# Kernel optimization log

Hardware: AMD Instinct MI355X
Metric: run time of the kernel (lower is better)

## Reference

```python
import jax, jax.numpy as jnp
import numpy as np

B, T, C = 2, 2048, 2048
H = 16
HD = C // H
MLP_DIM = 4 * C
EPS = 1e-5


def rmsnorm(x):
    return x * jax.lax.rsqrt(jnp.mean(x * x, axis=-1, keepdims=True) + EPS)


def setup_inputs() -> dict:
    key = jax.random.key(0)
    ks = jax.random.split(key, 7)
    s = 0.02
    return {
        "x": jax.random.normal(ks[0], (B, T, C), dtype=jnp.float32),
        "wq": jax.random.normal(ks[1], (C, C), dtype=jnp.float32) * s,
        "wk": jax.random.normal(ks[2], (C, C), dtype=jnp.float32) * s,
        "wv": jax.random.normal(ks[3], (C, C), dtype=jnp.float32) * s,
        "wo": jax.random.normal(ks[4], (C, C), dtype=jnp.float32) * s,
        "fc1": jax.random.normal(ks[5], (MLP_DIM, C), dtype=jnp.float32) * s,
        "fc2": jax.random.normal(ks[6], (C, MLP_DIM), dtype=jnp.float32) * s,
    }


def reference(x, wq, wk, wv, wo, fc1, fc2):
    # --- attention sub-block (pre-norm) ---
    h = rmsnorm(x)
    # nn.Linear applies x @ W.T
    q = (h @ wq.T).reshape(B, T, H, HD).transpose(0, 2, 1, 3)  # [B,H,T,HD]
    k = (h @ wk.T).reshape(B, T, H, HD).transpose(0, 2, 1, 3)
    v = (h @ wv.T).reshape(B, T, H, HD).transpose(0, 2, 1, 3)
    scale = 1.0 / np.sqrt(HD)
    scores = jnp.einsum("bhqd,bhkd->bhqk", q, k) * scale
    causal_mask = jnp.triu(jnp.full((T, T), -jnp.inf, dtype=scores.dtype), k=1)
    scores = scores + causal_mask
    attn = jax.nn.softmax(scores, axis=-1)
    out = jnp.einsum("bhqk,bhkd->bhqd", attn, v)
    out = out.transpose(0, 2, 1, 3).reshape(B, T, C)
    x = x + out @ wo.T
    # --- MLP sub-block (squared ReLU) ---
    h = rmsnorm(x)
    m = h @ fc1.T
    m = jnp.square(jax.nn.relu(m))
    x = x + m @ fc2.T
    return x
```

## Files before the change

### kernel.cpp

```cpp
#include <hip/hip_runtime.h>


typedef __bf16 bf16x8 __attribute__((ext_vector_type(8)));
typedef __bf16 bf16x4 __attribute__((ext_vector_type(4)));
typedef float  f32x4  __attribute__((ext_vector_type(4)));

static __device__ __forceinline__ __bf16 tobf(float f) { return (__bf16)f; }

static __device__ __forceinline__ void async_copy16(const void* g, void* l) {
    __builtin_amdgcn_global_load_lds(
        (const __attribute__((address_space(1))) void*)g,
        (__attribute__((address_space(3))) void*)l, 16, 0, 0);
}

#define LGKM0_FENCE()  asm volatile("s_waitcnt lgkmcnt(0)" ::: "memory")
#define VMCNT8_FENCE() asm volatile("s_waitcnt vmcnt(8)" ::: "memory")

__global__ void detect_dtype_kernel(const unsigned short* __restrict__ xh,
                                    int* __restrict__ flag) {
    int t = threadIdx.x;
    unsigned short u = xh[2 * t];
    int e = (u >> 7) & 0xFF;
    bool outlier = (e < 100) || (e > 131);
    unsigned long long m = __ballot(outlier);
    if (t == 0) *flag = (__popcll(m) >= 16) ? 1 : 0;
}

__global__ __launch_bounds__(256) void convert_w4(
    const void* __restrict__ w0, const void* __restrict__ w1,
    const void* __restrict__ w2, const void* __restrict__ w3,
    __bf16* __restrict__ dqkvo, const int* __restrict__ flagp) {
    constexpr size_t CC = (size_t)2048 * 2048;
    const int y = blockIdx.y;
    size_t i = ((size_t)blockIdx.x * 256 + threadIdx.x) * 8;
    const void* s = (y == 0) ? w0 : (y == 1) ? w1 : (y == 2) ? w2 : w3;
    __bf16* d = dqkvo + (size_t)y * CC;
    if (*flagp != 0) {
        const float4* sp = (const float4*)((const float*)s + i);
        float4 a = sp[0], b = sp[1];
        bf16x8 o = {tobf(a.x), tobf(a.y), tobf(a.z), tobf(a.w),
                    tobf(b.x), tobf(b.y), tobf(b.z), tobf(b.w)};
        *(bf16x8*)(d + i) = o;
    } else {
        *(bf16x8*)(d + i) = *(const bf16x8*)((const __bf16*)s + i);
    }
}

__global__ __launch_bounds__(256) void convert_w1(
    const void* __restrict__ src, __bf16* __restrict__ dst,
    const int* __restrict__ flagp) {
    size_t i = ((size_t)blockIdx.x * 256 + threadIdx.x) * 8;
    if (*flagp != 0) {
        const float4* sp = (const float4*)((const float*)src + i);
        float4 a = sp[0], b = sp[1];
        bf16x8 o = {tobf(a.x), tobf(a.y), tobf(a.z), tobf(a.w),
                    tobf(b.x), tobf(b.y), tobf(b.z), tobf(b.w)};
        *(bf16x8*)(dst + i) = o;
    } else {
        *(bf16x8*)(dst + i) = *(const bf16x8*)((const __bf16*)src + i);
    }
}

template <int SRC>
__global__ __launch_bounds__(256) void rmsnorm_kernel(
    const void* __restrict__ xp, __bf16* __restrict__ h,
    const int* __restrict__ flagp) {
    constexpr int C = 2048;
    const int row = blockIdx.x, t = threadIdx.x;
    float vals[8];
    bool f32in = (SRC == 1) || (*flagp != 0);
    if (f32in) {
        const float4* xr = (const float4*)((const float*)xp + (size_t)row * C);
        float4 a = xr[2 * t], b = xr[2 * t + 1];
        vals[0] = a.x; vals[1] = a.y; vals[2] = a.z; vals[3] = a.w;
        vals[4] = b.x; vals[5] = b.y; vals[6] = b.z; vals[7] = b.w;
    } else {
        bf16x8 a = *((const bf16x8*)((const __bf16*)xp + (size_t)row * C) + t);
#pragma unroll
        for (int j = 0; j < 8; ++j) vals[j] = (float)a[j];
    }
    float ss = 0.f;
#pragma unroll
    for (int j = 0; j < 8; ++j) ss += vals[j] * vals[j];
#pragma unroll
    for (int off = 32; off > 0; off >>= 1) ss += __shfl_down(ss, off);
    __shared__ float red[4];
    if ((t & 63) == 0) red[t >> 6] = ss;
    __syncthreads();
    float mean = (red[0] + red[1] + red[2] + red[3]) * (1.0f / C);
    float sc = rsqrtf(mean + 1e-5f);
    bf16x8 o;
#pragma unroll
    for (int j = 0; j < 8; ++j) o[j] = tobf(vals[j] * sc);
    *((bf16x8*)(h + (size_t)row * C) + t) = o;
}

static __device__ __forceinline__ void gemm_core_256(
    const __bf16* __restrict__ A, const __bf16* __restrict__ W,
    int m0, int n0, int K,
    __bf16 (*As)[256][64], __bf16 (*Bs)[256][64], f32x4 (&acc)[8][4]) {
    const int tid = threadIdx.x;
    const int wave = tid >> 6, lane = tid & 63;
    const int lr = lane & 15, lq = lane >> 4;
    const int wm = wave >> 2, wn = wave & 3;
    const int sx = lr & 7;
    const int NT = K >> 6;

    int off[4], lo[4];
#pragma unroll
    for (int i = 0; i < 4; ++i) {
        int c = i * 512 + tid;
        int row = c >> 3;
        off[i] = row * K + (((c & 7) ^ (row & 7)) * 8);
        lo[i] = (c & ~63) * 8;
    }

    const f32x4 zero = {0.f, 0.f, 0.f, 0.f};
#pragma unroll
    for (int m = 0; m < 8; ++m)
#pragma unroll
        for (int n = 0; n < 4; ++n) acc[m][n] = zero;

#pragma unroll
    for (int pt = 0; pt < 2; ++pt) {
        const __bf16* ga = A + (size_t)m0 * K + pt * 64;
        const __bf16* gb = W + (size_t)n0 * K + pt * 64;
#pragma unroll
        for (int i = 0; i < 4; ++i)
            async_copy16(ga + off[i], &As[pt][0][0] + lo[i]);
#pragma unroll
        for (int i = 0; i < 4; ++i)
            async_copy16(gb + off[i], &Bs[pt][0][0] + lo[i]);
    }
    VMCNT8_FENCE();
    __builtin_amdgcn_s_barrier();

    for (int t = 0; t < NT; ++t) {
        const int bi = t & 1;
        const __bf16 (*Ac)[64] = As[bi];
        const __bf16 (*Bc)[64] = Bs[bi];
        const int ts = (t + 2 < NT) ? t + 2 : NT - 1;
        const __bf16* gAt = A + (size_t)m0 * K + (size_t)ts * 64;
        const __bf16* gBt = W + (size_t)n0 * K + (size_t)ts * 64;

        bf16x8 a0[4][2], a1[4][2], b0[2][2], b1[2][2];

#pragma unroll
        for (int m = 0; m < 4; ++m)
#pragma unroll
            for (int kk = 0; kk < 2; ++kk)
                a0[m][kk] = *(const bf16x8*)
                    &Ac[wm * 128 + m * 16 + lr][((kk * 4 + lq) ^ sx) * 8];
#pragma unroll
        for (int n = 0; n < 2; ++n)
#pragma unroll
            for (int kk = 0; kk < 2; ++kk)
                b0[n][kk] = *(const bf16x8*)
                    &Bc[wn * 64 + n * 16 + lr][((kk * 4 + lq) ^ sx) * 8];
        __builtin_amdgcn_s_barrier();
        LGKM0_FENCE();
        __builtin_amdgcn_s_setprio(1);
#pragma unroll
        for (int m = 0; m < 4; ++m)
#pragma unroll
            for (int n = 0; n < 2; ++n)
#pragma unroll
                for (int kk = 0; kk < 2; ++kk)
                    acc[m][n] = __builtin_amdgcn_mfma_f32_16x16x32_bf16(
                        a0[m][kk], b0[n][kk], acc[m][n], 0, 0, 0);
        __builtin_amdgcn_s_setprio(0);
        __builtin_amdgcn_s_barrier();

#pragma unroll
        for (int m = 0; m < 4; ++m)
#pragma unroll
            for (int kk = 0; kk < 2; ++kk)
                a1[m][kk] = *(const bf16x8*)
                    &Ac[wm * 128 + (m + 4) * 16 + lr][((kk * 4 + lq) ^ sx) * 8];
        __builtin_amdgcn_s_barrier();
        LGKM0_FENCE();
        __builtin_amdgcn_s_setprio(1);
#pragma unroll
        for (int m = 0; m < 4; ++m)
#pragma unroll
            for (int n = 0; n < 2; ++n)
#pragma unroll
                for (int kk = 0; kk < 2; ++kk)
                    acc[m + 4][n] = __builtin_amdgcn_mfma_f32_16x16x32_bf16(
                        a1[m][kk], b0[n][kk], acc[m + 4][n], 0, 0, 0);
        __builtin_amdgcn_s_setprio(0);
        __builtin_amdgcn_s_barrier();

#pragma unroll
        for (int n = 0; n < 2; ++n)
#pragma unroll
            for (int kk = 0; kk < 2; ++kk)
                b1[n][kk] = *(const bf16x8*)
                    &Bc[wn * 64 + (n + 2) * 16 + lr][((kk * 4 + lq) ^ sx) * 8];
#pragma unroll
        for (int i = 0; i < 4; ++i)
            async_copy16(gAt + off[i], &As[bi][0][0] + lo[i]);
        __builtin_amdgcn_s_barrier();
        LGKM0_FENCE();
        __builtin_amdgcn_s_setprio(1);
#pragma unroll
        for (int m = 0; m < 4; ++m)
#pragma unroll
            for (int n = 0; n < 2; ++n)
#pragma unroll
                for (int kk = 0; kk < 2; ++kk)
                    acc[m + 4][n + 2] = __builtin_amdgcn_mfma_f32_16x16x32_bf16(
                        a1[m][kk], b1[n][kk], acc[m + 4][n + 2], 0, 0, 0);
        __builtin_amdgcn_s_setprio(0);
        __builtin_amdgcn_s_barrier();

#pragma unroll
        for (int i = 0; i < 4; ++i)
            async_copy16(gBt + off[i], &Bs[bi][0][0] + lo[i]);
        __builtin_amdgcn_s_barrier();
        __builtin_amdgcn_s_setprio(1);
#pragma unroll
        for (int m = 0; m < 4; ++m)
#pragma unroll
            for (int n = 0; n < 2; ++n)
#pragma unroll
                for (int kk = 0; kk < 2; ++kk)
                    acc[m][n + 2] = __builtin_amdgcn_mfma_f32_16x16x32_bf16(
                        a0[m][kk], b1[n][kk], acc[m][n + 2], 0, 0, 0);
        __builtin_amdgcn_s_setprio(0);
        VMCNT8_FENCE();
        __builtin_amdgcn_s_barrier();
    }
}

template <int EPI>
__global__ __launch_bounds__(512, 1) void gemm256_nt(
    const __bf16* __restrict__ A, const __bf16* __restrict__ W,
    void* __restrict__ outp, const void* __restrict__ resp,
    int M, int N, int K, const int* __restrict__ flagp) {
    __shared__ __align__(16) __bf16 As[2][256][64];
    __shared__ __align__(16) __bf16 Bs[2][256][64];
    const int tid = threadIdx.x;
    const int wave = tid >> 6, lane = tid & 63;
    const int lr = lane & 15, lq = lane >> 4;
    const int wm = wave >> 2, wn = wave & 3;
    const int m0 = blockIdx.y * 256, n0 = blockIdx.x * 256;

    f32x4 acc[8][4];
    gemm_core_256(A, W, m0, n0, K, As, Bs, acc);

    const bool f32 = (EPI == 2) ? false : (*flagp != 0);
#pragma unroll
    for (int m = 0; m < 8; ++m)
#pragma unroll
        for (int n = 0; n < 4; ++n)
#pragma unroll
            for (int r = 0; r < 4; ++r) {
                int row = m0 + wm * 128 + m * 16 + lq * 4 + r;
                int col = n0 + wn * 64 + n * 16 + lr;
                size_t o = (size_t)row * N + col;
                float v = acc[m][n][r];
                if (EPI == 2) {
                    float rv = v > 0.f ? v : 0.f;
                    ((__bf16*)outp)[o] = tobf(rv * rv);
                } else if (EPI == 5) {
                    float res = f32 ? ((const float*)resp)[o]
                                    : (float)((const __bf16*)resp)[o];
                    ((float*)outp)[o] = v + res;
                } else {
                    float ov = v + ((const float*)resp)[o];
                    if (f32) ((float*)outp)[o] = ov;
                    else     ((__bf16*)outp)[o] = tobf(ov);
                }
            }
}

__global__ __launch_bounds__(512, 1) void gemm256_qkv(
    const __bf16* __restrict__ A, const __bf16* __restrict__ Wall,
    __bf16* __restrict__ qout, __bf16* __restrict__ kout,
    __bf16* __restrict__ vtout) {
    constexpr int N = 2048, K = 2048;
    constexpr float kQScale = 1.4426950408889634f * 0.08838834764831845f;
    __shared__ __align__(16) __bf16 As[2][256][64];
    __shared__ __align__(16) __bf16 Bs[2][256][64];
    const int tid = threadIdx.x;
    const int wave = tid >> 6, lane = tid & 63;
    const int lr = lane & 15, lq = lane >> 4;
    const int wm = wave >> 2, wn = wave & 3;
    const int which = blockIdx.x >> 3;
    const int m0 = blockIdx.y * 256, n0 = (blockIdx.x & 7) * 256;
    const __bf16* W = Wall + (size_t)which * N * K;

    f32x4 acc[8][4];
    gemm_core_256(A, W, m0, n0, K, As, Bs, acc);

    if (which < 2) {
        __bf16* outp = (which == 0) ? qout : kout;
        const float sc = (which == 0) ? kQScale : 1.0f;
#pragma unroll
        for (int m = 0; m < 8; ++m)
#pragma unroll
            for (int n = 0; n < 4; ++n)
#pragma unroll
                for (int r = 0; r < 4; ++r) {
                    int row = m0 + wm * 128 + m * 16 + lq * 4 + r;
                    int col = n0 + wn * 64 + n * 16 + lr;
                    outp[(size_t)row * N + col] = tobf(acc[m][n][r] * sc);
                }
    } else {
#pragma unroll
        for (int m = 0; m < 8; ++m)
#pragma unroll
            for (int n = 0; n < 4; ++n) {
                int t0 = m0 + wm * 128 + m * 16 + lq * 4;
                int b  = t0 >> 11, tt = t0 & 2047;
                int col = n0 + wn * 64 + n * 16 + lr;
                bf16x4 p = {tobf(acc[m][n][0]), tobf(acc[m][n][1]),
                            tobf(acc[m][n][2]), tobf(acc[m][n][3])};
                *(bf16x4*)(vtout + (((size_t)(b * 2048 + col)) << 11) + tt) = p;
            }
    }
}

static __device__ __forceinline__ void gemm_core_128(
    const __bf16* __restrict__ A, const __bf16* __restrict__ W,
    int m0, int n0, int K,
    __bf16 (*As)[64], __bf16 (*Bs)[64], f32x4 (&acc)[4][4]) {
    const int t = threadIdx.x;
    const int wave = t >> 6, lane = t & 63;
    const int lr = lane & 15, lq = lane >> 4;
    const int wm = wave & 1, wn = wave >> 1;

    const __bf16* gA[4];
    const __bf16* gB[4];
    int lo[4];
#pragma unroll
    for (int i = 0; i < 4; ++i) {
        int c = i * 256 + t;
        int row = c >> 3;
        int sl = (c & 7) ^ (row & 7);
        gA[i] = A + (size_t)(m0 + row) * K + sl * 8;
        gB[i] = W + (size_t)(n0 + row) * K + sl * 8;
        lo[i] = (c & ~63) * 8;
    }
    const int sx = lr & 7;

    const f32x4 zero = {0.f, 0.f, 0.f, 0.f};
#pragma unroll
    for (int i = 0; i < 4; ++i)
#pragma unroll
        for (int j = 0; j < 4; ++j) acc[i][j] = zero;

    for (int k0 = 0; k0 < K; k0 += 64) {
#pragma unroll
        for (int i = 0; i < 4; ++i) {
            async_copy16(gA[i] + k0, &As[0][0] + lo[i]);
            async_copy16(gB[i] + k0, &Bs[0][0] + lo[i]);
        }
        __syncthreads();
#pragma unroll
        for (int kk = 0; kk < 2; ++kk) {
            const int sp = ((kk * 4 + lq) ^ sx) * 8;
            bf16x8 a[4], b[4];
#pragma unroll
            for (int ii = 0; ii < 4; ++ii) {
                a[ii] = *(const bf16x8*)&As[wm * 64 + ii * 16 + lr][sp];
                b[ii] = *(const bf16x8*)&Bs[wn * 64 + ii * 16 + lr][sp];
            }
#pragma unroll
            for (int ii = 0; ii < 4; ++ii)
#pragma unroll
                for (int jj = 0; jj < 4; ++jj)
                    acc[ii][jj] = __builtin_amdgcn_mfma_f32_16x16x32_bf16(
                        a[ii], b[jj], acc[ii][jj], 0, 0, 0);
        }
        __syncthreads();
    }
}

template <int EPI>
__global__ __launch_bounds__(256) void gemm_nt(
    const __bf16* __restrict__ A, const __bf16* __restrict__ W,
    void* __restrict__ outp, const void* __restrict__ resp,
    int M, int N, int K, const int* __restrict__ flagp) {
    __shared__ __align__(16) __bf16 As[128][64];
    __shared__ __align__(16) __bf16 Bs[128][64];
    const int t = threadIdx.x;
    const int wave = t >> 6, lane = t & 63;
    const int lr = lane & 15, lq = lane >> 4;
    const int wm = wave & 1, wn = wave >> 1;
    const int m0 = blockIdx.y * 128, n0 = blockIdx.x * 128;

    f32x4 acc[4][4];
    gemm_core_128(A, W, m0, n0, K, As, Bs, acc);

    const bool f32 = (*flagp != 0);
#pragma unroll
    for (int i = 0; i < 4; ++i)
#pragma unroll
        for (int j = 0; j < 4; ++j)
#pragma unroll
            for (int r = 0; r < 4; ++r) {
                int row = m0 + wm * 64 + i * 16 + lq * 4 + r;
                int col = n0 + wn * 64 + j * 16 + lr;
                size_t o = (size_t)row * N + col;
                float v = acc[i][j][r];
                if (EPI == 5) {
                    float res = f32 ? ((const float*)resp)[o]
                                    : (float)((const __bf16*)resp)[o];
                    ((float*)outp)[o] = v + res;
                } else {
                    float ov = v + ((const float*)resp)[o];
                    if (f32) ((float*)outp)[o] = ov;
                    else     ((__bf16*)outp)[o] = tobf(ov);
                }
            }
}

__global__ __launch_bounds__(256) void attn_kernel(
    const __bf16* __restrict__ Q, const __bf16* __restrict__ K,
    const __bf16* __restrict__ Vt, __bf16* __restrict__ O) {
    constexpr int T = 2048, C = 2048, HD = 128;
    __shared__ __align__(16) __bf16 Ks[64][136];
    __shared__ __align__(16) __bf16 Vts[128][72];
    __shared__ __align__(16) __bf16 Ps[4][16][72];
    const int t = threadIdx.x, w = t >> 6, lane = t & 63;
    const int lr = lane & 15, lq = lane >> 4;
    const int b = blockIdx.z, h = blockIdx.y;
    const __bf16* vtb = Vt + ((size_t)(b * 2048 + h * 128) << 11);
    const f32x4 zero = {0.f, 0.f, 0.f, 0.f};

    bf16x8 ones;
#pragma unroll
    for (int j = 0; j < 8; ++j) ones[j] = (lr == 0) ? (__bf16)1.0f : (__bf16)0.0f;

    for (int pass = 0; pass < 2; ++pass) {
        const int qblk = (pass == 0) ? blockIdx.x : 31 - blockIdx.x;
        const int q0 = qblk * 64;

        const int qrow = q0 + w * 16 + lr;
        const __bf16* qb = Q + (size_t)(b * T + qrow) * C + h * HD;
        bf16x8 qf[4];
#pragma unroll
        for (int s = 0; s < 4; ++s)
            qf[s] = *(const bf16x8*)(qb + s * 32 + lq * 8);

        f32x4 oacc[8], lacc = zero;
#pragma unroll
        for (int nc = 0; nc < 8; ++nc) oacc[nc] = zero;
        float m_i[4] = {-3e38f, -3e38f, -3e38f, -3e38f};

        for (int kb = 0; kb <= qblk; ++kb) {
            const int k00 = kb * 64;
#pragma unroll
            for (int i = 0; i < 4; ++i) {
                int c = t + 256 * i;
                int r = c >> 4, col = (c & 15) * 8;
                *(bf16x8*)&Ks[r][col] =
                    *(const bf16x8*)(K + (size_t)(b * T + k00 + r) * C + h * HD + col);
            }
#pragma unroll
            for (int i = 0; i < 4; ++i) {
                int c = t + 256 * i;
                int r = c >> 3, cg = (c & 7) * 8;
                *(bf16x8*)&Vts[r][cg] =
                    *(const bf16x8*)(vtb + ((size_t)r << 11) + k00 + cg);
            }
            __syncthreads();

            float pv[4][4];
#pragma unroll
            for (int jc = 0; jc < 4; ++jc) {
                f32x4 s = zero;
#pragma unroll
                for (int ks = 0; ks < 4; ++ks) {
                    bf16x8 kf = *(const bf16x8*)&Ks[jc * 16 + lr][ks * 32 + lq * 8];
                    s = __builtin_amdgcn_mfma_f32_16x16x32_bf16(qf[ks], kf, s, 0, 0, 0);
                }
#pragma unroll
                for (int r = 0; r < 4; ++r) pv[jc][r] = s[r];
            }
            if (kb == qblk) {
#pragma unroll
                for (int jc = 0; jc < 4; ++jc)
#pragma unroll
                    for (int r = 0; r < 4; ++r)
                        if (jc * 16 + lr > w * 16 + lq * 4 + r) pv[jc][r] = -3e38f;
            }
            float rmax[4];
#pragma unroll
            for (int r = 0; r < 4; ++r)
                rmax[r] = fmaxf(fmaxf(pv[0][r], pv[1][r]), fmaxf(pv[2][r], pv[3][r]));
#pragma unroll
            for (int off = 1; off < 16; off <<= 1)
#pragma unroll
                for (int r = 0; r < 4; ++r)
                    rmax[r] = fmaxf(rmax[r], __shfl_xor(rmax[r], off));
            float alpha[4];
#pragma unroll
            for (int r = 0; r < 4; ++r) {
                float mn = fmaxf(m_i[r], rmax[r]);
                alpha[r] = exp2f(m_i[r] - mn);
                m_i[r] = mn;
            }
#pragma unroll
            for (int jc = 0; jc < 4; ++jc)
#pragma unroll
                for (int r = 0; r < 4; ++r)
                    Ps[w][lq * 4 + r][jc * 16 + lr] = tobf(exp2f(pv[jc][r] - m_i[r]));
#pragma unroll
            for (int nc = 0; nc < 8; ++nc)
#pragma unroll
                for (int r = 0; r < 4; ++r) oacc[nc][r] *= alpha[r];
#pragma unroll
            for (int r = 0; r < 4; ++r) lacc[r] *= alpha[r];
            __syncthreads();

#pragma unroll
            for (int s2 = 0; s2 < 2; ++s2) {
                bf16x8 pa = *(const bf16x8*)&Ps[w][lr][s2 * 32 + lq * 8];
#pragma unroll
                for (int nc = 0; nc < 8; ++nc) {
                    bf16x8 vf = *(const bf16x8*)&Vts[nc * 16 + lr][s2 * 32 + lq * 8];
                    oacc[nc] = __builtin_amdgcn_mfma_f32_16x16x32_bf16(
                        pa, vf, oacc[nc], 0, 0, 0);
                }
                lacc = __builtin_amdgcn_mfma_f32_16x16x32_bf16(pa, ones, lacc, 0, 0, 0);
            }
            __syncthreads();
        }

        float inv[4];
#pragma unroll
        for (int r = 0; r < 4; ++r) inv[r] = 1.0f / __shfl(lacc[r], lane & 48);
#pragma unroll
        for (int nc = 0; nc < 8; ++nc)
#pragma unroll
            for (int r = 0; r < 4; ++r) {
                int row = q0 + w * 16 + lq * 4 + r;
                O[(size_t)(b * T + row) * C + h * HD + nc * 16 + lr] =
                    tobf(oacc[nc][r] * inv[r]);
            }
        __syncthreads();
    }
}

extern "C" void kernel_launch(void* const* d_in, const int* in_sizes, int n_in,
                              void* d_out, int out_size, void* d_ws, size_t ws_size,
                              hipStream_t stream) {
    const void* x   = d_in[0];
    const void* wq  = d_in[1];
    const void* wk  = d_in[2];
    const void* wv  = d_in[3];
    const void* wo  = d_in[4];
    const void* fc1 = d_in[5];
    const void* fc2 = d_in[6];
    constexpr int Bv = 2, Tv = 2048, Cv = 2048, Hv = 16, MLP = 8192;
    constexpr int M = Bv * Tv;
    constexpr size_t NE = (size_t)M * Cv;
    constexpr size_t CC = (size_t)Cv * Cv;

    char* ws = (char*)d_ws;
    int*    flag = (int*)ws;
    __bf16* h    = (__bf16*)(ws + 256);
    __bf16* qb   = h  + NE;
    __bf16* kb   = qb + NE;
    __bf16* vt   = kb + NE;
    __bf16* ao   = vt + NE;
    float*  x1   = (float*)(ao + NE);
    __bf16* mm   = (__bf16*)(x1 + NE);
    __bf16* wqkvob = mm;
    __bf16* fc1b   = qb;
    __bf16* fc2b   = vt;

    detect_dtype_kernel<<<1, 64, 0, stream>>>((const unsigned short*)x, flag);

    convert_w4<<<dim3(2048, 4), 256, 0, stream>>>(wq, wk, wv, wo, wqkvob, flag);

    rmsnorm_kernel<0><<<M, 256, 0, stream>>>(x, h, flag);

    gemm256_qkv<<<dim3(24, 16), 512, 0, stream>>>(h, wqkvob, qb, kb, vt);

    attn_kernel<<<dim3(16, Hv, Bv), 256, 0, stream>>>(qb, kb, vt, ao);

    convert_w1<<<8192, 256, 0, stream>>>(fc1, fc1b, flag);

    gemm_nt<5><<<dim3(16, 32), 256, 0, stream>>>(ao, wqkvob + 3 * CC, x1, x,
                                                 M, Cv, Cv, flag);

    convert_w1<<<8192, 256, 0, stream>>>(fc2, fc2b, flag);

    rmsnorm_kernel<1><<<M, 256, 0, stream>>>(x1, h, flag);

    gemm256_nt<2><<<dim3(32, 16), 512, 0, stream>>>(h, fc1b, mm, nullptr,
                                                    M, MLP, Cv, flag);

    gemm_nt<6><<<dim3(16, 32), 256, 0, stream>>>(mm, fc2b, d_out, x1,
                                                 M, Cv, MLP, flag);
}
```

Before: 800.8 us.

## Templatize 8-phase GEMM core and use 128x256 tiles for QKV, out-proj, fc2

Generalizes the pipelined 256x256 GEMM core into a template over the M tile height, so a 128x256 variant can share the same double-buffered async-copy and MFMA schedule. The QKV projection now uses 128x256 tiles, giving 768 blocks instead of 384 for better CU balance. The out-projection and fc2 GEMMs move from the simple single-buffered 128x128 kernel to this pipelined 128x256 kernel. The trade-off is less operand reuse per block than 256x256 and more blocks to schedule.

```diff
diff --git a/kernel.cpp b/kernel.cpp
--- a/kernel.cpp
+++ b/kernel.cpp
@@ -14,7 +14,6 @@
 }
 
 #define LGKM0_FENCE()  asm volatile("s_waitcnt lgkmcnt(0)" ::: "memory")
-#define VMCNT8_FENCE() asm volatile("s_waitcnt vmcnt(8)" ::: "memory")
 
 __global__ void detect_dtype_kernel(const unsigned short* __restrict__ xh,
                                     int* __restrict__ flag) {
@@ -95,10 +94,14 @@
     *((bf16x8*)(h + (size_t)row * C) + t) = o;
 }
 
-static __device__ __forceinline__ void gemm_core_256(
+template <int MH>
+static __device__ __forceinline__ void gemm_core_8ph(
     const __bf16* __restrict__ A, const __bf16* __restrict__ W,
-    int m0, int n0, int K,
-    __bf16 (*As)[256][64], __bf16 (*Bs)[256][64], f32x4 (&acc)[8][4]) {
+    int m0, int n0, int K, __bf16* __restrict__ AsB, __bf16* __restrict__ BsB,
+    f32x4 (&acc)[2 * MH][4]) {
+    constexpr int BM = 64 * MH;
+    constexpr int ASTRIDE = BM * 64;
+    constexpr int BSTRIDE = 256 * 64;
     const int tid = threadIdx.x;
     const int wave = tid >> 6, lane = tid & 63;
     const int lr = lane & 15, lq = lane >> 4;
@@ -106,18 +109,25 @@
     const int sx = lr & 7;
     const int NT = K >> 6;
 
-    int off[4], lo[4];
+    int offA[MH], loA[MH], offB[4], loB[4];
+#pragma unroll
+    for (int i = 0; i < MH; ++i) {
+        int c = i * 512 + tid;
+        int row = c >> 3;
+        offA[i] = row * K + (((c & 7) ^ (row & 7)) * 8);
+        loA[i] = (c & ~63) * 8;
+    }
 #pragma unroll
     for (int i = 0; i < 4; ++i) {
         int c = i * 512 + tid;
         int row = c >> 3;
-        off[i] = row * K + (((c & 7) ^ (row & 7)) * 8);
-        lo[i] = (c & ~63) * 8;
+        offB[i] = row * K + (((c & 7) ^ (row & 7)) * 8);
+        loB[i] = (c & ~63) * 8;
     }
 
     const f32x4 zero = {0.f, 0.f, 0.f, 0.f};
 #pragma unroll
-    for (int m = 0; m < 8; ++m)
+    for (int m = 0; m < 2 * MH; ++m)
 #pragma unroll
         for (int n = 0; n < 4; ++n) acc[m][n] = zero;
 
@@ -125,43 +135,46 @@
     for (int pt = 0; pt < 2; ++pt) {
         const __bf16* ga = A + (size_t)m0 * K + pt * 64;
         const __bf16* gb = W + (size_t)n0 * K + pt * 64;
-#pragma unroll
-        for (int i = 0; i < 4; ++i)
-            async_copy16(ga + off[i], &As[pt][0][0] + lo[i]);
-#pragma unroll
-        for (int i = 0; i < 4; ++i)
-            async_copy16(gb + off[i], &Bs[pt][0][0] + lo[i]);
-    }
-    VMCNT8_FENCE();
+        __bf16* la = AsB + pt * ASTRIDE;
+        __bf16* lb = BsB + pt * BSTRIDE;
+#pragma unroll
+        for (int i = 0; i < MH; ++i) async_copy16(ga + offA[i], la + loA[i]);
+#pragma unroll
+        for (int i = 0; i < 4; ++i)  async_copy16(gb + offB[i], lb + loB[i]);
+    }
+    if constexpr (MH == 4) asm volatile("s_waitcnt vmcnt(8)" ::: "memory");
+    else                   asm volatile("s_waitcnt vmcnt(6)" ::: "memory");
     __builtin_amdgcn_s_barrier();
 
     for (int t = 0; t < NT; ++t) {
         const int bi = t & 1;
-        const __bf16 (*Ac)[64] = As[bi];
-        const __bf16 (*Bc)[64] = Bs[bi];
+        const __bf16* Ac = AsB + bi * ASTRIDE;
+        const __bf16* Bc = BsB + bi * BSTRIDE;
         const int ts = (t + 2 < NT) ? t + 2 : NT - 1;
         const __bf16* gAt = A + (size_t)m0 * K + (size_t)ts * 64;
         const __bf16* gBt = W + (size_t)n0 * K + (size_t)ts * 64;
 
-        bf16x8 a0[4][2], a1[4][2], b0[2][2], b1[2][2];
-
-#pragma unroll
-        for (int m = 0; m < 4; ++m)
+        bf16x8 a0[MH][2], a1[MH][2], b0[2][2], b1[2][2];
+
+#pragma unroll
+        for (int m = 0; m < MH; ++m)
 #pragma unroll
             for (int kk = 0; kk < 2; ++kk)
                 a0[m][kk] = *(const bf16x8*)
-                    &Ac[wm * 128 + m * 16 + lr][((kk * 4 + lq) ^ sx) * 8];
+                    &Ac[(wm * (32 * MH) + m * 16 + lr) * 64 +
+                        ((kk * 4 + lq) ^ sx) * 8];
 #pragma unroll
         for (int n = 0; n < 2; ++n)
 #pragma unroll
             for (int kk = 0; kk < 2; ++kk)
                 b0[n][kk] = *(const bf16x8*)
-                    &Bc[wn * 64 + n * 16 + lr][((kk * 4 + lq) ^ sx) * 8];
+                    &Bc[(wn * 64 + n * 16 + lr) * 64 +
+                        ((kk * 4 + lq) ^ sx) * 8];
         __builtin_amdgcn_s_barrier();
         LGKM0_FENCE();
         __builtin_amdgcn_s_setprio(1);
 #pragma unroll
-        for (int m = 0; m < 4; ++m)
+        for (int m = 0; m < MH; ++m)
 #pragma unroll
             for (int n = 0; n < 2; ++n)
 #pragma unroll
@@ -172,22 +185,23 @@
         __builtin_amdgcn_s_barrier();
 
 #pragma unroll
-        for (int m = 0; m < 4; ++m)
+        for (int m = 0; m < MH; ++m)
 #pragma unroll
             for (int kk = 0; kk < 2; ++kk)
                 a1[m][kk] = *(const bf16x8*)
-                    &Ac[wm * 128 + (m + 4) * 16 + lr][((kk * 4 + lq) ^ sx) * 8];
+                    &Ac[(wm * (32 * MH) + (m + MH) * 16 + lr) * 64 +
+                        ((kk * 4 + lq) ^ sx) * 8];
         __builtin_amdgcn_s_barrier();
         LGKM0_FENCE();
         __builtin_amdgcn_s_setprio(1);
 #pragma unroll
-        for (int m = 0; m < 4; ++m)
+        for (int m = 0; m < MH; ++m)
 #pragma unroll
             for (int n = 0; n < 2; ++n)
 #pragma unroll
                 for (int kk = 0; kk < 2; ++kk)
-                    acc[m + 4][n] = __builtin_amdgcn_mfma_f32_16x16x32_bf16(
-                        a1[m][kk], b0[n][kk], acc[m + 4][n], 0, 0, 0);
+                    acc[m + MH][n] = __builtin_amdgcn_mfma_f32_16x16x32_bf16(
+                        a1[m][kk], b0[n][kk], acc[m + MH][n], 0, 0, 0);
         __builtin_amdgcn_s_setprio(0);
         __builtin_amdgcn_s_barrier();
 
@@ -196,31 +210,32 @@
 #pragma unroll
             for (int kk = 0; kk < 2; ++kk)
                 b1[n][kk] = *(const bf16x8*)
-                    &Bc[wn * 64 + (n + 2) * 16 + lr][((kk * 4 + lq) ^ sx) * 8];
-#pragma unroll
-        for (int i = 0; i < 4; ++i)
-            async_copy16(gAt + off[i], &As[bi][0][0] + lo[i]);
+                    &Bc[(wn * 64 + (n + 2) * 16 + lr) * 64 +
+                        ((kk * 4 + lq) ^ sx) * 8];
+#pragma unroll
+        for (int i = 0; i < MH; ++i)
+            async_copy16(gAt + offA[i], AsB + bi * ASTRIDE + loA[i]);
         __builtin_amdgcn_s_barrier();
         LGKM0_FENCE();
         __builtin_amdgcn_s_setprio(1);
 #pragma unroll
-        for (int m = 0; m < 4; ++m)
+        for (int m = 0; m < MH; ++m)
 #pragma unroll
             for (int n = 0; n < 2; ++n)
 #pragma unroll
                 for (int kk = 0; kk < 2; ++kk)
-                    acc[m + 4][n + 2] = __builtin_amdgcn_mfma_f32_16x16x32_bf16(
-                        a1[m][kk], b1[n][kk], acc[m + 4][n + 2], 0, 0, 0);
+                    acc[m + MH][n + 2] = __builtin_amdgcn_mfma_f32_16x16x32_bf16(
+                        a1[m][kk], b1[n][kk], acc[m + MH][n + 2], 0, 0, 0);
         __builtin_amdgcn_s_setprio(0);
         __builtin_amdgcn_s_barrier();
 
 #pragma unroll
         for (int i = 0; i < 4; ++i)
-            async_copy16(gBt + off[i], &Bs[bi][0][0] + lo[i]);
+            async_copy16(gBt + offB[i], BsB + bi * BSTRIDE + loB[i]);
         __builtin_amdgcn_s_barrier();
         __builtin_amdgcn_s_setprio(1);
 #pragma unroll
-        for (int m = 0; m < 4; ++m)
+        for (int m = 0; m < MH; ++m)
 #pragma unroll
             for (int n = 0; n < 2; ++n)
 #pragma unroll
@@ -228,7 +243,8 @@
                     acc[m][n + 2] = __builtin_amdgcn_mfma_f32_16x16x32_bf16(
                         a0[m][kk], b1[n][kk], acc[m][n + 2], 0, 0, 0);
         __builtin_amdgcn_s_setprio(0);
-        VMCNT8_FENCE();
+        if constexpr (MH == 4) asm volatile("s_waitcnt vmcnt(8)" ::: "memory");
+        else                   asm volatile("s_waitcnt vmcnt(6)" ::: "memory");
         __builtin_amdgcn_s_barrier();
     }
 }
@@ -247,7 +263,7 @@
     const int m0 = blockIdx.y * 256, n0 = blockIdx.x * 256;
 
     f32x4 acc[8][4];
-    gemm_core_256(A, W, m0, n0, K, As, Bs, acc);
+    gemm_core_8ph<4>(A, W, m0, n0, K, &As[0][0][0], &Bs[0][0][0], acc);
 
     const bool f32 = (EPI == 2) ? false : (*flagp != 0);
 #pragma unroll
@@ -275,136 +291,33 @@
             }
 }
 
-__global__ __launch_bounds__(512, 1) void gemm256_qkv(
-    const __bf16* __restrict__ A, const __bf16* __restrict__ Wall,
-    __bf16* __restrict__ qout, __bf16* __restrict__ kout,
-    __bf16* __restrict__ vtout) {
-    constexpr int N = 2048, K = 2048;
-    constexpr float kQScale = 1.4426950408889634f * 0.08838834764831845f;
-    __shared__ __align__(16) __bf16 As[2][256][64];
+template <int EPI>
+__global__ __launch_bounds__(512, 1) void gemm128_nt(
+    const __bf16* __restrict__ A, const __bf16* __restrict__ W,
+    void* __restrict__ outp, const void* __restrict__ resp,
+    int M, int N, int K, const int* __restrict__ flagp) {
+    __shared__ __align__(16) __bf16 As[2][128][64];
     __shared__ __align__(16) __bf16 Bs[2][256][64];
     const int tid = threadIdx.x;
     const int wave = tid >> 6, lane = tid & 63;
     const int lr = lane & 15, lq = lane >> 4;
     const int wm = wave >> 2, wn = wave & 3;
-    const int which = blockIdx.x >> 3;
-    const int m0 = blockIdx.y * 256, n0 = (blockIdx.x & 7) * 256;
-    const __bf16* W = Wall + (size_t)which * N * K;
-
-    f32x4 acc[8][4];
-    gemm_core_256(A, W, m0, n0, K, As, Bs, acc);
-
-    if (which < 2) {
-        __bf16* outp = (which == 0) ? qout : kout;
-        const float sc = (which == 0) ? kQScale : 1.0f;
-#pragma unroll
-        for (int m = 0; m < 8; ++m)
-#pragma unroll
-            for (int n = 0; n < 4; ++n)
-#pragma unroll
-                for (int r = 0; r < 4; ++r) {
-                    int row = m0 + wm * 128 + m * 16 + lq * 4 + r;
-                    int col = n0 + wn * 64 + n * 16 + lr;
-                    outp[(size_t)row * N + col] = tobf(acc[m][n][r] * sc);
-                }
-    } else {
-#pragma unroll
-        for (int m = 0; m < 8; ++m)
-#pragma unroll
-            for (int n = 0; n < 4; ++n) {
-                int t0 = m0 + wm * 128 + m * 16 + lq * 4;
-                int b  = t0 >> 11, tt = t0 & 2047;
+    const int m0 = blockIdx.y * 128, n0 = blockIdx.x * 256;
+
+    f32x4 acc[4][4];
+    gemm_core_8ph<2>(A, W, m0, n0, K, &As[0][0][0], &Bs[0][0][0], acc);
+
+    const bool f32 = (*flagp != 0);
+#pragma unroll
+    for (int m = 0; m < 4; ++m)
+#pragma unroll
+        for (int n = 0; n < 4; ++n)
+#pragma unroll
+            for (int r = 0; r < 4; ++r) {
+                int row = m0 + wm * 64 + m * 16 + lq * 4 + r;
                 int col = n0 + wn * 64 + n * 16 + lr;
-                bf16x4 p = {tobf(acc[m][n][0]), tobf(acc[m][n][1]),
-                            tobf(acc[m][n][2]), tobf(acc[m][n][3])};
-                *(bf16x4*)(vtout + (((size_t)(b * 2048 + col)) << 11) + tt) = p;
-            }
-    }
-}
-
-static __device__ __forceinline__ void gemm_core_128(
-    const __bf16* __restrict__ A, const __bf16* __restrict__ W,
-    int m0, int n0, int K,
-    __bf16 (*As)[64], __bf16 (*Bs)[64], f32x4 (&acc)[4][4]) {
-    const int t = threadIdx.x;
-    const int wave = t >> 6, lane = t & 63;
-    const int lr = lane & 15, lq = lane >> 4;
-    const int wm = wave & 1, wn = wave >> 1;
-
-    const __bf16* gA[4];
-    const __bf16* gB[4];
-    int lo[4];
-#pragma unroll
-    for (int i = 0; i < 4; ++i) {
-        int c = i * 256 + t;
-        int row = c >> 3;
-        int sl = (c & 7) ^ (row & 7);
-        gA[i] = A + (size_t)(m0 + row) * K + sl * 8;
-        gB[i] = W + (size_t)(n0 + row) * K + sl * 8;
-        lo[i] = (c & ~63) * 8;
-    }
-    const int sx = lr & 7;
-
-    const f32x4 zero = {0.f, 0.f, 0.f, 0.f};
-#pragma unroll
-    for (int i = 0; i < 4; ++i)
-#pragma unroll
-        for (int j = 0; j < 4; ++j) acc[i][j] = zero;
-
-    for (int k0 = 0; k0 < K; k0 += 64) {
-#pragma unroll
-        for (int i = 0; i < 4; ++i) {
-            async_copy16(gA[i] + k0, &As[0][0] + lo[i]);
-            async_copy16(gB[i] + k0, &Bs[0][0] + lo[i]);
-        }
-        __syncthreads();
-#pragma unroll
-        for (int kk = 0; kk < 2; ++kk) {
-            const int sp = ((kk * 4 + lq) ^ sx) * 8;
-            bf16x8 a[4], b[4];
-#pragma unroll
-            for (int ii = 0; ii < 4; ++ii) {
-                a[ii] = *(const bf16x8*)&As[wm * 64 + ii * 16 + lr][sp];
-                b[ii] = *(const bf16x8*)&Bs[wn * 64 + ii * 16 + lr][sp];
-            }
-#pragma unroll
-            for (int ii = 0; ii < 4; ++ii)
-#pragma unroll
-                for (int jj = 0; jj < 4; ++jj)
-                    acc[ii][jj] = __builtin_amdgcn_mfma_f32_16x16x32_bf16(
-                        a[ii], b[jj], acc[ii][jj], 0, 0, 0);
-        }
-        __syncthreads();
-    }
-}
-
-template <int EPI>
-__global__ __launch_bounds__(256) void gemm_nt(
-    const __bf16* __restrict__ A, const __bf16* __restrict__ W,
-    void* __restrict__ outp, const void* __restrict__ resp,
-    int M, int N, int K, const int* __restrict__ flagp) {
-    __shared__ __align__(16) __bf16 As[128][64];
-    __shared__ __align__(16) __bf16 Bs[128][64];
-    const int t = threadIdx.x;
-    const int wave = t >> 6, lane = t & 63;
-    const int lr = lane & 15, lq = lane >> 4;
-    const int wm = wave & 1, wn = wave >> 1;
-    const int m0 = blockIdx.y * 128, n0 = blockIdx.x * 128;
-
-    f32x4 acc[4][4];
-    gemm_core_128(A, W, m0, n0, K, As, Bs, acc);
-
-    const bool f32 = (*flagp != 0);
-#pragma unroll
-    for (int i = 0; i < 4; ++i)
-#pragma unroll
-        for (int j = 0; j < 4; ++j)
-#pragma unroll
-            for (int r = 0; r < 4; ++r) {
-                int row = m0 + wm * 64 + i * 16 + lq * 4 + r;
-                int col = n0 + wn * 64 + j * 16 + lr;
                 size_t o = (size_t)row * N + col;
-                float v = acc[i][j][r];
+                float v = acc[m][n][r];
                 if (EPI == 5) {
                     float res = f32 ? ((const float*)resp)[o]
                                     : (float)((const __bf16*)resp)[o];
@@ -415,6 +328,53 @@
                     else     ((__bf16*)outp)[o] = tobf(ov);
                 }
             }
+}
+
+__global__ __launch_bounds__(512, 1) void gemm_qkv128(
+    const __bf16* __restrict__ A, const __bf16* __restrict__ Wall,
+    __bf16* __restrict__ qout, __bf16* __restrict__ kout,
+    __bf16* __restrict__ vtout) {
+    constexpr int N = 2048, K = 2048;
+    constexpr float kQScale = 1.4426950408889634f * 0.08838834764831845f;
+    __shared__ __align__(16) __bf16 As[2][128][64];
+    __shared__ __align__(16) __bf16 Bs[2][256][64];
+    const int tid = threadIdx.x;
+    const int wave = tid >> 6, lane = tid & 63;
+    const int lr = lane & 15, lq = lane >> 4;
+    const int wm = wave >> 2, wn = wave & 3;
+    const int which = blockIdx.x >> 3;
+    const int m0 = blockIdx.y * 128, n0 = (blockIdx.x & 7) * 256;
+    const __bf16* W = Wall + (size_t)which * N * K;
+
+    f32x4 acc[4][4];
+    gemm_core_8ph<2>(A, W, m0, n0, K, &As[0][0][0], &Bs[0][0][0], acc);
+
+    if (which < 2) {
+        __bf16* outp = (which == 0) ? qout : kout;
+        const float sc = (which == 0) ? kQScale : 1.0f;
+#pragma unroll
+        for (int m = 0; m < 4; ++m)
+#pragma unroll
+            for (int n = 0; n < 4; ++n)
+#pragma unroll
+                for (int r = 0; r < 4; ++r) {
+                    int row = m0 + wm * 64 + m * 16 + lq * 4 + r;
+                    int col = n0 + wn * 64 + n * 16 + lr;
+                    outp[(size_t)row * N + col] = tobf(acc[m][n][r] * sc);
+                }
+    } else {
+#pragma unroll
+        for (int m = 0; m < 4; ++m)
+#pragma unroll
+            for (int n = 0; n < 4; ++n) {
+                int t0 = m0 + wm * 64 + m * 16 + lq * 4;
+                int b  = t0 >> 11, tt = t0 & 2047;
+                int col = n0 + wn * 64 + n * 16 + lr;
+                bf16x4 p = {tobf(acc[m][n][0]), tobf(acc[m][n][1]),
+                            tobf(acc[m][n][2]), tobf(acc[m][n][3])};
+                *(bf16x4*)(vtout + (((size_t)(b * 2048 + col)) << 11) + tt) = p;
+            }
+    }
 }
 
 __global__ __launch_bounds__(256) void attn_kernel(
@@ -579,14 +539,14 @@
 
     rmsnorm_kernel<0><<<M, 256, 0, stream>>>(x, h, flag);
 
-    gemm256_qkv<<<dim3(24, 16), 512, 0, stream>>>(h, wqkvob, qb, kb, vt);
+    gemm_qkv128<<<dim3(24, 32), 512, 0, stream>>>(h, wqkvob, qb, kb, vt);
 
     attn_kernel<<<dim3(16, Hv, Bv), 256, 0, stream>>>(qb, kb, vt, ao);
 
     convert_w1<<<8192, 256, 0, stream>>>(fc1, fc1b, flag);
 
-    gemm_nt<5><<<dim3(16, 32), 256, 0, stream>>>(ao, wqkvob + 3 * CC, x1, x,
-                                                 M, Cv, Cv, flag);
+    gemm128_nt<5><<<dim3(8, 32), 512, 0, stream>>>(ao, wqkvob + 3 * CC, x1, x,
+                                                   M, Cv, Cv, flag);
 
     convert_w1<<<8192, 256, 0, stream>>>(fc2, fc2b, flag);
 
@@ -595,6 +555,6 @@
     gemm256_nt<2><<<dim3(32, 16), 512, 0, stream>>>(h, fc1b, mm, nullptr,
                                                     M, MLP, Cv, flag);
 
-    gemm_nt<6><<<dim3(16, 32), 256, 0, stream>>>(mm, fc2b, d_out, x1,
-                                                 M, Cv, MLP, flag);
-}
+    gemm128_nt<6><<<dim3(8, 32), 512, 0, stream>>>(mm, fc2b, d_out, x1,
+                                                   M, Cv, MLP, flag);
+}
```

Measured after the change: 825.2 us. +3.1%, slower.

## Double-buffer 128-tile GEMM core and use it for the QKV projection

Applied to the files above, without the earlier changes.

Adds a double-buffered 128x128 GEMM core that prefetches the next K tile with async global-to-LDS copies while the current tile feeds the MFMAs, waiting only on the older loads. gemm_nt now uses this core instead of the single-buffered one, and the QKV projection moves from the 256x256/512-thread kernel to the 128-tile kernel with 4x as many blocks. The aim is to hide load latency and to fill more CUs on the QKV GEMM. The cost is twice the LDS per block and less data reuse per block on QKV.

```diff
diff --git a/kernel.cpp b/kernel.cpp
--- a/kernel.cpp
+++ b/kernel.cpp
@@ -15,6 +15,8 @@
 
 #define LGKM0_FENCE()  asm volatile("s_waitcnt lgkmcnt(0)" ::: "memory")
 #define VMCNT8_FENCE() asm volatile("s_waitcnt vmcnt(8)" ::: "memory")
+#define VMCNT0_FENCE() asm volatile("s_waitcnt vmcnt(0)" ::: "memory")
+#define CFENCE()       asm volatile("" ::: "memory")
 
 __global__ void detect_dtype_kernel(const unsigned short* __restrict__ xh,
                                     int* __restrict__ flag) {
@@ -95,6 +97,168 @@
     *((bf16x8*)(h + (size_t)row * C) + t) = o;
 }
 
+static __device__ __forceinline__ void gemm_core_128pf(
+    const __bf16* __restrict__ A, const __bf16* __restrict__ W,
+    int m0, int n0, int K,
+    __bf16 (*As)[128][64], __bf16 (*Bs)[128][64], f32x4 (&acc)[4][4]) {
+    const int t = threadIdx.x;
+    const int wave = t >> 6, lane = t & 63;
+    const int lr = lane & 15, lq = lane >> 4;
+    const int wm = wave & 1, wn = wave >> 1;
+    const int sx = lr & 7;
+    const int NT = K >> 6;
+
+    const __bf16* gA[4];
+    const __bf16* gB[4];
+    int lo[4];
+#pragma unroll
+    for (int i = 0; i < 4; ++i) {
+        int c = i * 256 + t;
+        int row = c >> 3;
+        int sl = (c & 7) ^ (row & 7);
+        gA[i] = A + (size_t)(m0 + row) * K + sl * 8;
+        gB[i] = W + (size_t)(n0 + row) * K + sl * 8;
+        lo[i] = (c & ~63) * 8;
+    }
+
+    const f32x4 zero = {0.f, 0.f, 0.f, 0.f};
+#pragma unroll
+    for (int i = 0; i < 4; ++i)
+#pragma unroll
+        for (int j = 0; j < 4; ++j) acc[i][j] = zero;
+
+#pragma unroll
+    for (int i = 0; i < 4; ++i) {
+        async_copy16(gA[i], &As[0][0][0] + lo[i]);
+        async_copy16(gB[i], &Bs[0][0][0] + lo[i]);
+    }
+
+    for (int tt = 0; tt < NT; ++tt) {
+        const int cur = tt & 1;
+        if (tt + 1 < NT) {
+            const int k1 = (tt + 1) * 64;
+#pragma unroll
+            for (int i = 0; i < 4; ++i) {
+                async_copy16(gA[i] + k1, &As[cur ^ 1][0][0] + lo[i]);
+                async_copy16(gB[i] + k1, &Bs[cur ^ 1][0][0] + lo[i]);
+            }
+            VMCNT8_FENCE();
+        } else {
+            VMCNT0_FENCE();
+        }
+        __builtin_amdgcn_s_barrier();
+        CFENCE();
+
+        bf16x8 a[4][2], b[4][2];
+#pragma unroll
+        for (int kk = 0; kk < 2; ++kk) {
+            const int sp = ((kk * 4 + lq) ^ sx) * 8;
+#pragma unroll
+            for (int ii = 0; ii < 4; ++ii) {
+                a[ii][kk] = *(const bf16x8*)&As[cur][wm * 64 + ii * 16 + lr][sp];
+                b[ii][kk] = *(const bf16x8*)&Bs[cur][wn * 64 + ii * 16 + lr][sp];
+            }
+        }
+#pragma unroll
+        for (int ii = 0; ii < 4; ++ii)
+#pragma unroll
+            for (int jj = 0; jj < 4; ++jj)
+#pragma unroll
+                for (int kk = 0; kk < 2; ++kk)
+                    acc[ii][jj] = __builtin_amdgcn_mfma_f32_16x16x32_bf16(
+                        a[ii][kk], b[jj][kk], acc[ii][jj], 0, 0, 0);
+        CFENCE();
+        __builtin_amdgcn_s_barrier();
+        CFENCE();
+    }
+}
+
+template <int EPI>
+__global__ __launch_bounds__(256) void gemm_nt(
+    const __bf16* __restrict__ A, const __bf16* __restrict__ W,
+    void* __restrict__ outp, const void* __restrict__ resp,
+    int M, int N, int K, const int* __restrict__ flagp) {
+    __shared__ __align__(16) __bf16 As[2][128][64];
+    __shared__ __align__(16) __bf16 Bs[2][128][64];
+    const int t = threadIdx.x;
+    const int wave = t >> 6, lane = t & 63;
+    const int lr = lane & 15, lq = lane >> 4;
+    const int wm = wave & 1, wn = wave >> 1;
+    const int m0 = blockIdx.y * 128, n0 = blockIdx.x * 128;
+
+    f32x4 acc[4][4];
+    gemm_core_128pf(A, W, m0, n0, K, As, Bs, acc);
+
+    const bool f32 = (*flagp != 0);
+#pragma unroll
+    for (int i = 0; i < 4; ++i)
+#pragma unroll
+        for (int j = 0; j < 4; ++j)
+#pragma unroll
+            for (int r = 0; r < 4; ++r) {
+                int row = m0 + wm * 64 + i * 16 + lq * 4 + r;
+                int col = n0 + wn * 64 + j * 16 + lr;
+                size_t o = (size_t)row * N + col;
+                float v = acc[i][j][r];
+                if (EPI == 5) {
+                    float res = f32 ? ((const float*)resp)[o]
+                                    : (float)((const __bf16*)resp)[o];
+                    ((float*)outp)[o] = v + res;
+                } else {
+                    float ov = v + ((const float*)resp)[o];
+                    if (f32) ((float*)outp)[o] = ov;
+                    else     ((__bf16*)outp)[o] = tobf(ov);
+                }
+            }
+}
+
+__global__ __launch_bounds__(256) void gemm_qkv(
+    const __bf16* __restrict__ A, const __bf16* __restrict__ Wall,
+    __bf16* __restrict__ qout, __bf16* __restrict__ kout,
+    __bf16* __restrict__ vtout) {
+    constexpr int N = 2048, K = 2048;
+    constexpr float kQScale = 1.4426950408889634f * 0.08838834764831845f;
+    __shared__ __align__(16) __bf16 As[2][128][64];
+    __shared__ __align__(16) __bf16 Bs[2][128][64];
+    const int t = threadIdx.x;
+    const int wave = t >> 6, lane = t & 63;
+    const int lr = lane & 15, lq = lane >> 4;
+    const int wm = wave & 1, wn = wave >> 1;
+    const int which = blockIdx.x >> 4;
+    const int m0 = blockIdx.y * 128, n0 = (blockIdx.x & 15) * 128;
+    const __bf16* W = Wall + (size_t)which * N * K;
+
+    f32x4 acc[4][4];
+    gemm_core_128pf(A, W, m0, n0, K, As, Bs, acc);
+
+    if (which < 2) {
+        __bf16* outp = (which == 0) ? qout : kout;
+        const float sc = (which == 0) ? kQScale : 1.0f;
+#pragma unroll
+        for (int i = 0; i < 4; ++i)
+#pragma unroll
+            for (int j = 0; j < 4; ++j)
+#pragma unroll
+                for (int r = 0; r < 4; ++r) {
+                    int row = m0 + wm * 64 + i * 16 + lq * 4 + r;
+                    int col = n0 + wn * 64 + j * 16 + lr;
+                    outp[(size_t)row * N + col] = tobf(acc[i][j][r] * sc);
+                }
+    } else {
+#pragma unroll
+        for (int i = 0; i < 4; ++i)
+#pragma unroll
+            for (int j = 0; j < 4; ++j) {
+                int t0 = m0 + wm * 64 + i * 16 + lq * 4;
+                int b  = t0 >> 11, tt = t0 & 2047;
+                int col = n0 + wn * 64 + j * 16 + lr;
+                bf16x4 p = {tobf(acc[i][j][0]), tobf(acc[i][j][1]),
+                            tobf(acc[i][j][2]), tobf(acc[i][j][3])};
+                *(bf16x4*)(vtout + (((size_t)(b * 2048 + col)) << 11) + tt) = p;
+            }
+    }
+}
+
 static __device__ __forceinline__ void gemm_core_256(
     const __bf16* __restrict__ A, const __bf16* __restrict__ W,
     int m0, int n0, int K,
@@ -275,148 +439,6 @@
             }
 }
 
-__global__ __launch_bounds__(512, 1) void gemm256_qkv(
-    const __bf16* __restrict__ A, const __bf16* __restrict__ Wall,
-    __bf16* __restrict__ qout, __bf16* __restrict__ kout,
-    __bf16* __restrict__ vtout) {
-    constexpr int N = 2048, K = 2048;
-    constexpr float kQScale = 1.4426950408889634f * 0.08838834764831845f;
-    __shared__ __align__(16) __bf16 As[2][256][64];
-    __shared__ __align__(16) __bf16 Bs[2][256][64];
-    const int tid = threadIdx.x;
-    const int wave = tid >> 6, lane = tid & 63;
-    const int lr = lane & 15, lq = lane >> 4;
-    const int wm = wave >> 2, wn = wave & 3;
-    const int which = blockIdx.x >> 3;
-    const int m0 = blockIdx.y * 256, n0 = (blockIdx.x & 7) * 256;
-    const __bf16* W = Wall + (size_t)which * N * K;
-
-    f32x4 acc[8][4];
-    gemm_core_256(A, W, m0, n0, K, As, Bs, acc);
-
-    if (which < 2) {
-        __bf16* outp = (which == 0) ? qout : kout;
-        const float sc = (which == 0) ? kQScale : 1.0f;
-#pragma unroll
-        for (int m = 0; m < 8; ++m)
-#pragma unroll
-            for (int n = 0; n < 4; ++n)
-#pragma unroll
-                for (int r = 0; r < 4; ++r) {
-                    int row = m0 + wm * 128 + m * 16 + lq * 4 + r;
-                    int col = n0 + wn * 64 + n * 16 + lr;
-                    outp[(size_t)row * N + col] = tobf(acc[m][n][r] * sc);
-                }
-    } else {
-#pragma unroll
-        for (int m = 0; m < 8; ++m)
-#pragma unroll
-            for (int n = 0; n < 4; ++n) {
-                int t0 = m0 + wm * 128 + m * 16 + lq * 4;
-                int b  = t0 >> 11, tt = t0 & 2047;
-                int col = n0 + wn * 64 + n * 16 + lr;
-                bf16x4 p = {tobf(acc[m][n][0]), tobf(acc[m][n][1]),
-                            tobf(acc[m][n][2]), tobf(acc[m][n][3])};
-                *(bf16x4*)(vtout + (((size_t)(b * 2048 + col)) << 11) + tt) = p;
-            }
-    }
-}
-
-static __device__ __forceinline__ void gemm_core_128(
-    const __bf16* __restrict__ A, const __bf16* __restrict__ W,
-    int m0, int n0, int K,
-    __bf16 (*As)[64], __bf16 (*Bs)[64], f32x4 (&acc)[4][4]) {
-    const int t = threadIdx.x;
-    const int wave = t >> 6, lane = t & 63;
-    const int lr = lane & 15, lq = lane >> 4;
-    const int wm = wave & 1, wn = wave >> 1;
-
-    const __bf16* gA[4];
-    const __bf16* gB[4];
-    int lo[4];
-#pragma unroll
-    for (int i = 0; i < 4; ++i) {
-        int c = i * 256 + t;
-        int row = c >> 3;
-        int sl = (c & 7) ^ (row & 7);
-        gA[i] = A + (size_t)(m0 + row) * K + sl * 8;
-        gB[i] = W + (size_t)(n0 + row) * K + sl * 8;
-        lo[i] = (c & ~63) * 8;
-    }
-    const int sx = lr & 7;
-
-    const f32x4 zero = {0.f, 0.f, 0.f, 0.f};
-#pragma unroll
-    for (int i = 0; i < 4; ++i)
-#pragma unroll
-        for (int j = 0; j < 4; ++j) acc[i][j] = zero;
-
-    for (int k0 = 0; k0 < K; k0 += 64) {
-#pragma unroll
-        for (int i = 0; i < 4; ++i) {
-            async_copy16(gA[i] + k0, &As[0][0] + lo[i]);
-            async_copy16(gB[i] + k0, &Bs[0][0] + lo[i]);
-        }
-        __syncthreads();
-#pragma unroll
-        for (int kk = 0; kk < 2; ++kk) {
-            const int sp = ((kk * 4 + lq) ^ sx) * 8;
-            bf16x8 a[4], b[4];
-#pragma unroll
-            for (int ii = 0; ii < 4; ++ii) {
-                a[ii] = *(const bf16x8*)&As[wm * 64 + ii * 16 + lr][sp];
-                b[ii] = *(const bf16x8*)&Bs[wn * 64 + ii * 16 + lr][sp];
-            }
-#pragma unroll
-            for (int ii = 0; ii < 4; ++ii)
-#pragma unroll
-                for (int jj = 0; jj < 4; ++jj)
-                    acc[ii][jj] = __builtin_amdgcn_mfma_f32_16x16x32_bf16(
-                        a[ii], b[jj], acc[ii][jj], 0, 0, 0);
-        }
-        __syncthreads();
-    }
-}
-
-template <int EPI>
-__global__ __launch_bounds__(256) void gemm_nt(
-    const __bf16* __restrict__ A, const __bf16* __restrict__ W,
-    void* __restrict__ outp, const void* __restrict__ resp,
-    int M, int N, int K, const int* __restrict__ flagp) {
-    __shared__ __align__(16) __bf16 As[128][64];
-    __shared__ __align__(16) __bf16 Bs[128][64];
-    const int t = threadIdx.x;
-    const int wave = t >> 6, lane = t & 63;
-    const int lr = lane & 15, lq = lane >> 4;
-    const int wm = wave & 1, wn = wave >> 1;
-    const int m0 = blockIdx.y * 128, n0 = blockIdx.x * 128;
-
-    f32x4 acc[4][4];
-    gemm_core_128(A, W, m0, n0, K, As, Bs, acc);
-
-    const bool f32 = (*flagp != 0);
-#pragma unroll
-    for (int i = 0; i < 4; ++i)
-#pragma unroll
-        for (int j = 0; j < 4; ++j)
-#pragma unroll
-            for (int r = 0; r < 4; ++r) {
-                int row = m0 + wm * 64 + i * 16 + lq * 4 + r;
-                int col = n0 + wn * 64 + j * 16 + lr;
-                size_t o = (size_t)row * N + col;
-                float v = acc[i][j][r];
-                if (EPI == 5) {
-                    float res = f32 ? ((const float*)resp)[o]
-                                    : (float)((const __bf16*)resp)[o];
-                    ((float*)outp)[o] = v + res;
-                } else {
-                    float ov = v + ((const float*)resp)[o];
-                    if (f32) ((float*)outp)[o] = ov;
-                    else     ((__bf16*)outp)[o] = tobf(ov);
-                }
-            }
-}
-
 __global__ __launch_bounds__(256) void attn_kernel(
     const __bf16* __restrict__ Q, const __bf16* __restrict__ K,
     const __bf16* __restrict__ Vt, __bf16* __restrict__ O) {
@@ -579,7 +601,7 @@
 
     rmsnorm_kernel<0><<<M, 256, 0, stream>>>(x, h, flag);
 
-    gemm256_qkv<<<dim3(24, 16), 512, 0, stream>>>(h, wqkvob, qb, kb, vt);
+    gemm_qkv<<<dim3(48, 32), 256, 0, stream>>>(h, wqkvob, qb, kb, vt);
 
     attn_kernel<<<dim3(16, Hv, Bv), 256, 0, stream>>>(qb, kb, vt, ao);
 
```

Result: faster. 772.4 us (-3.5%).
